# Kernel optimization log

Measured on AMD Instinct MI355X. Metric: run time of the kernel, lower is better.

The kernel has to match this reference:

```python
import jax, jax.numpy as jnp
import numpy as np

K_UP = 5
UP = 2
KS = 3
C_IN = 256


def pixel_shuffle(x, r):
    N, C, H, W = x.shape
    x = x.reshape(N, C // (r * r), r, r, H, W)
    return x.transpose(0, 1, 4, 2, 5, 3).reshape(N, C // (r * r), H * r, W * r)


def conv2d(x, w, b, pad):
    y = jax.lax.conv_general_dilated(
        x, w, window_strides=(1, 1), padding=[(pad, pad), (pad, pad)],
        dimension_numbers=('NCHW', 'OIHW', 'NCHW'))
    return y + b[None, :, None, None]


def setup_inputs() -> dict:
    key = jax.random.key(0)
    ks = jax.random.split(key, 7)
    C = C_IN
    Cd = C // 2
    Ce = UP * UP * K_UP * K_UP  # 100
    x = jax.random.normal(ks[0], (4, C, 64, 64), dtype=jnp.float32)
    # kaiming-normal-ish inits, biases small uniform (torch default)
    w_down = jax.random.normal(ks[1], (Cd, C, 1, 1), dtype=jnp.float32) * np.sqrt(2.0 / C)
    b_down = jax.random.uniform(ks[2], (Cd,), dtype=jnp.float32, minval=-0.05, maxval=0.05)
    w_enc = jax.random.normal(ks[3], (Ce, Cd, KS, KS), dtype=jnp.float32) * np.sqrt(2.0 / (Cd * KS * KS))
    b_enc = jax.random.uniform(ks[4], (Ce,), dtype=jnp.float32, minval=-0.05, maxval=0.05)
    w_out = jax.random.normal(ks[5], (C, C, 1, 1), dtype=jnp.float32) * np.sqrt(2.0 / C)
    b_out = jax.random.uniform(ks[6], (C,), dtype=jnp.float32, minval=-0.05, maxval=0.05)
    return {"x": x, "w_down": w_down, "b_down": b_down, "w_enc": w_enc,
            "b_enc": b_enc, "w_out": w_out, "b_out": b_out}


def reference(x, w_down, b_down, w_enc, b_enc, w_out, b_out):
    N, C, H, W = x.shape
    k2 = K_UP * K_UP  # 25
    u2 = UP * UP      # 4
    # kernel prediction branch
    kt = conv2d(x, w_down, b_down, 0)
    kt = conv2d(kt, w_enc, b_enc, KS // 2)
    kt = pixel_shuffle(kt, UP)              # (N, 25, H*UP, W*UP)
    kt = jax.nn.softmax(kt, axis=1)
    # unfold(2,UP,UP).unfold(3,UP,UP) -> (N,25,H,W,UP,UP) -> (N,H,W,25,UP*UP)
    kt = kt.reshape(N, k2, H, UP, W, UP).transpose(0, 2, 4, 1, 3, 5)
    kt = kt.reshape(N, H, W, k2, u2)
    # feature patches: pad then gather k_up x k_up window per pixel
    pad = K_UP // 2
    xp = jnp.pad(x, ((0, 0), (0, 0), (pad, pad), (pad, pad)))
    patches = jnp.stack(
        [xp[:, :, i:i + H, j:j + W] for i in range(K_UP) for j in range(K_UP)],
        axis=-1)                            # (N, C, H, W, 25)
    # per-pixel weighted sum: (N,H,W,C,25) @ (N,H,W,25,u2)
    out = jnp.einsum('nchwk,nhwkp->nchwp', patches, kt)  # (N,C,H,W,u2)
    out = out.transpose(0, 1, 4, 2, 3).reshape(N, C * u2, H, W)
    out = pixel_shuffle(out, UP)            # (N, C, H*UP, W*UP)
    return conv2d(out, w_out, b_out, 0)
```

## Files before the change

kernel.cpp:

```cpp
#include <hip/hip_runtime.h>
#include <hip/hip_bf16.h>


#define NB    4
#define NPIX  4096

typedef short s16x8 __attribute__((ext_vector_type(8)));
typedef float f32x4 __attribute__((ext_vector_type(4)));

#define MFMA16(a, b, c) __builtin_amdgcn_mfma_f32_16x16x32_bf16((a), (b), (c), 0, 0, 0)

__device__ __forceinline__ ushort f2b(float f) {
    __hip_bfloat16 h = __float2bfloat16(f);
    return *(ushort*)&h;
}
__device__ __forceinline__ float b2f(ushort u) {
    unsigned v = ((unsigned)u) << 16;
    return *(float*)&v;
}

__global__ __launch_bounds__(256) void prep_kernel(
    const float* __restrict__ wd, const float* __restrict__ wo,
    const float* __restrict__ we,
    ushort* __restrict__ wcomb, ushort* __restrict__ wrb)
{
    int idx = blockIdx.x * 256 + threadIdx.x;
    if (idx < 98304) {
        float v = (idx < 32768) ? wd[idx] : wo[idx - 32768];
        wcomb[idx] = f2b(v);
    } else if (idx < 227328) {
        int i = idx - 98304;
        int co = i / 1152, k = i - co * 1152;
        int tap = k >> 7, c = k & 127;
        float v = (co < 100) ? we[(co * 128 + c) * 9 + tap] : 0.0f;
        wrb[i] = f2b(v);
    }
}

__global__ __launch_bounds__(512, 1) void dual_gemm_kernel(
    const float*  __restrict__ X,
    const ushort* __restrict__ Wcomb,
    const float*  __restrict__ b_down,
    ushort* __restrict__ T1t,
    ushort* __restrict__ XOt)
{
    __shared__ __attribute__((aligned(16))) ushort xs[64][264];
    const int n = blockIdx.y, p0 = blockIdx.x * 64;
    const int tid = threadIdx.x, lane = tid & 63, wid = tid >> 6;
    const int l15 = lane & 15, l4 = lane >> 4;
    const float* Xn = X + (size_t)n * 256 * NPIX + p0;

    {
        int c = tid >> 1, half = tid & 1;
        const float* src = Xn + (size_t)c * NPIX + half * 32;
        #pragma unroll
        for (int j = 0; j < 8; j++) {
            float4 v = *(const float4*)&src[j * 4];
            int pix = half * 32 + j * 4;
            xs[pix + 0][c] = f2b(v.x);
            xs[pix + 1][c] = f2b(v.y);
            xs[pix + 2][c] = f2b(v.z);
            xs[pix + 3][c] = f2b(v.w);
        }
    }
    __syncthreads();

    const int wp = wid >> 1;
    const int wc = wid & 1;
    const int crow = wc * 192;

    f32x4 acc[12] = {};
    #pragma unroll
    for (int ks = 0; ks < 8; ks++) {
        int k0 = ks * 32 + l4 * 8;
        s16x8 a = *(const s16x8*)&xs[wp * 16 + l15][k0];
        #pragma unroll
        for (int cf = 0; cf < 12; cf++) {
            s16x8 b = *(const s16x8*)&Wcomb[(size_t)(crow + cf * 16 + l15) * 256 + k0];
            acc[cf] = MFMA16(a, b, acc[cf]);
        }
    }

    #pragma unroll
    for (int cf = 0; cf < 12; cf++) {
        int cbase = crow + cf * 16;
        int c = cbase + l15;
        if (cbase < 128) {
            float bb = b_down[c];
            #pragma unroll
            for (int r = 0; r < 4; r++) {
                int pix = p0 + wp * 16 + l4 * 4 + r;
                T1t[(size_t)(n * NPIX + pix) * 128 + c] = f2b(acc[cf][r] + bb);
            }
        } else {
            int c2 = c - 128;
            #pragma unroll
            for (int r = 0; r < 4; r++) {
                int pix = p0 + wp * 16 + l4 * 4 + r;
                XOt[(size_t)(n * NPIX + pix) * 256 + c2] = f2b(acc[cf][r]);
            }
        }
    }
}

#define SMEM_A 27264
#define SMEM_TOTAL (SMEM_A + 74240)

__global__ __launch_bounds__(512, 1) void carafe_fused_kernel(
    const ushort* __restrict__ T1t,
    const ushort* __restrict__ Wr,
    const float*  __restrict__ Benc,
    const ushort* __restrict__ XOt,
    const float*  __restrict__ Bout,
    float* __restrict__ Z)
{
    __shared__ __attribute__((aligned(16))) char smem[SMEM_TOTAL];
    ushort (*hs)[136]   = (ushort(*)[136])smem;
    float  (*sm)[64][4] = (float(*)[64][4])smem;
    float  (*eld)[101]  = (float(*)[101])(smem + SMEM_A);
    float  (*xs)[145]   = (float(*)[145])(smem + SMEM_A);

    const int n = blockIdx.y, tile = blockIdx.x;
    const int h0 = (tile >> 3) * 8, w0 = (tile & 7) * 8;
    const int tid = threadIdx.x, lane = tid & 63, wid = tid >> 6;
    const int l15 = lane & 15, l4 = lane >> 4;

    for (int u = tid; u < 1600; u += 512) {
        int hp = u >> 4, ch = u & 15;
        int r = hp / 10, s = hp - r * 10;
        int gh = h0 - 1 + r, gw = w0 - 1 + s;
        s16x8 v = {};
        if ((unsigned)gh < 64u && (unsigned)gw < 64u)
            v = *(const s16x8*)&T1t[((size_t)n * NPIX + gh * 64 + gw) * 128 + ch * 8];
        *(s16x8*)&hs[hp][ch * 8] = v;
    }
    __syncthreads();

    if (wid < 4) {
        const int pl = wid * 16 + l15;
        const int ph = pl >> 3, pw = pl & 7;
        f32x4 acc[7] = {};
        for (int tap = 0; tap < 9; tap++) {
            int dy = tap / 3, dx = tap - dy * 3;
            int hp = (ph + dy) * 10 + pw + dx;
            const ushort* hrow = &hs[hp][l4 * 8];
            const ushort* wrow = &Wr[(size_t)l15 * 1152 + tap * 128 + l4 * 8];
            #pragma unroll
            for (int cb = 0; cb < 4; cb++) {
                s16x8 b = *(const s16x8*)&hrow[cb * 32];
                #pragma unroll
                for (int mf = 0; mf < 7; mf++) {
                    s16x8 a = *(const s16x8*)&wrow[(size_t)mf * 16 * 1152 + cb * 32];
                    acc[mf] = MFMA16(a, b, acc[mf]);
                }
            }
        }
        #pragma unroll
        for (int mf = 0; mf < 7; mf++) {
            #pragma unroll
            for (int r = 0; r < 4; r++) {
                int co = mf * 16 + l4 * 4 + r;
                if (co < 100) eld[pl][co] = acc[mf][r] + Benc[co];
            }
        }
    }
    __syncthreads();

    if (tid < 256) {
        int p = tid & 3, pix = tid >> 2;
        float v[25];
        float mx = -1e30f;
        #pragma unroll
        for (int k = 0; k < 25; k++) { v[k] = eld[pix][4 * k + p]; mx = fmaxf(mx, v[k]); }
        float ssum = 0.0f;
        #pragma unroll
        for (int k = 0; k < 25; k++) { v[k] = __expf(v[k] - mx); ssum += v[k]; }
        float inv = 1.0f / ssum;
        #pragma unroll
        for (int k = 0; k < 25; k++) sm[k][pix][p] = v[k] * inv;
    }
    __syncthreads();

    const int pix = tid & 63;
    const int og8 = tid >> 6;
    const int ph = pix >> 3, pw = pix & 7;
    const int cl = og8 >> 2;
    const int g  = og8 & 3;

    for (int it = 0; it < 2; it++) {
        for (int u = tid; u < 4608; u += 512) {
            int hp = u >> 5, cg = u & 31;
            int r = hp / 12, s = hp - r * 12;
            int gh = h0 - 2 + r, gw = w0 - 2 + s;
            float v0 = 0.f, v1 = 0.f, v2 = 0.f, v3 = 0.f;
            if ((unsigned)gh < 64u && (unsigned)gw < 64u) {
                ushort4 raw = *(const ushort4*)&XOt[((size_t)n * NPIX + gh * 64 + gw) * 256 + it * 128 + cg * 4];
                v0 = b2f(raw.x); v1 = b2f(raw.y); v2 = b2f(raw.z); v3 = b2f(raw.w);
            }
            xs[cg * 4 + 0][hp] = v0;
            xs[cg * 4 + 1][hp] = v1;
            xs[cg * 4 + 2][hp] = v2;
            xs[cg * 4 + 3][hp] = v3;
        }
        __syncthreads();

        float acc[16][4] = {};
        for (int k = 0; k < 25; k++) {
            int di = k / 5, dj = k - di * 5;
            float4 wv = *(const float4*)&sm[k][pix][0];
            int base = (ph + di) * 12 + pw + dj;
            #pragma unroll
            for (int i = 0; i < 16; i++) {
                float xv = xs[cl * 64 + g * 16 + i][base];
                acc[i][0] += xv * wv.x;
                acc[i][1] += xv * wv.y;
                acc[i][2] += xv * wv.z;
                acc[i][3] += xv * wv.w;
            }
        }

        const int gh = h0 + ph, gw = w0 + pw;
        const int oc = it * 2 + cl;
        #pragma unroll
        for (int i = 0; i < 16; i++) {
            int o = oc * 64 + g * 16 + i;
            float bb = Bout[o];
            float2 r0 = make_float2(acc[i][0] + bb, acc[i][1] + bb);
            float2 r1 = make_float2(acc[i][2] + bb, acc[i][3] + bb);
            size_t zb = (((size_t)n * 256 + o) * 128 + 2 * gh) * 128 + 2 * gw;
            *(float2*)&Z[zb]       = r0;
            *(float2*)&Z[zb + 128] = r1;
        }
        if (it == 0) __syncthreads();
    }
}

extern "C" void kernel_launch(void* const* d_in, const int* in_sizes, int n_in,
                              void* d_out, int out_size, void* d_ws, size_t ws_size,
                              hipStream_t stream) {
    const float* x      = (const float*)d_in[0];
    const float* w_down = (const float*)d_in[1];
    const float* b_down = (const float*)d_in[2];
    const float* w_enc  = (const float*)d_in[3];
    const float* b_enc  = (const float*)d_in[4];
    const float* w_out  = (const float*)d_in[5];
    const float* b_out  = (const float*)d_in[6];
    float* z = (float*)d_out;

    ushort* t1T   = (ushort*)d_ws;
    ushort* xoT   = t1T + 2097152;
    ushort* wcomb = xoT + 4194304;
    ushort* wrb   = wcomb + 98304;

    prep_kernel<<<888, 256, 0, stream>>>(w_down, w_out, w_enc, wcomb, wrb);
    dual_gemm_kernel<<<dim3(64, NB), 512, 0, stream>>>(x, wcomb, b_down, t1T, xoT);
    carafe_fused_kernel<<<dim3(64, NB), 512, 0, stream>>>(t1T, wrb, b_enc, xoT, b_out, z);
}
```

Before: 170.1 us.

## Split fused CARAFE kernel into conv-softmax and reassembly kernels for more blocks

The fused conv+softmax+reassembly kernel becomes two kernels: one computes the encoder conv and softmax and writes the softmax weights to global workspace, the other does the reassembly per 64-channel group over a 3D grid of 1024 blocks. The dual GEMM kernel is also retiled to 32-pixel, 256-thread blocks with two blocks per CU. The aim is to fill the GPU, since the old grid of 256 blocks of 512 threads left many CUs idle on this chip. In exchange it adds a global round trip for the softmax weights, an extra launch, and repeated loads of the weights by each channel group.

```diff
diff --git a/kernel.cpp b/kernel.cpp
--- a/kernel.cpp
+++ b/kernel.cpp
@@ -37,40 +37,37 @@
     }
 }
 
-__global__ __launch_bounds__(512, 1) void dual_gemm_kernel(
+__global__ __launch_bounds__(256, 2) void dual_gemm_kernel(
     const float*  __restrict__ X,
     const ushort* __restrict__ Wcomb,
     const float*  __restrict__ b_down,
     ushort* __restrict__ T1t,
     ushort* __restrict__ XOt)
 {
-    __shared__ __attribute__((aligned(16))) ushort xs[64][264];
-    const int n = blockIdx.y, p0 = blockIdx.x * 64;
+    __shared__ __attribute__((aligned(16))) ushort xs[32][264];
+    const int n = blockIdx.y, p0 = blockIdx.x * 32;
     const int tid = threadIdx.x, lane = tid & 63, wid = tid >> 6;
     const int l15 = lane & 15, l4 = lane >> 4;
-    const float* Xn = X + (size_t)n * 256 * NPIX + p0;
-
-    {
-        int c = tid >> 1, half = tid & 1;
-        const float* src = Xn + (size_t)c * NPIX + half * 32;
+
+    {
+        const float* src = X + (size_t)n * 256 * NPIX + (size_t)tid * NPIX + p0;
         #pragma unroll
         for (int j = 0; j < 8; j++) {
             float4 v = *(const float4*)&src[j * 4];
-            int pix = half * 32 + j * 4;
-            xs[pix + 0][c] = f2b(v.x);
-            xs[pix + 1][c] = f2b(v.y);
-            xs[pix + 2][c] = f2b(v.z);
-            xs[pix + 3][c] = f2b(v.w);
-        }
-    }
-    __syncthreads();
-
-    const int wp = wid >> 1;
-    const int wc = wid & 1;
+            xs[j * 4 + 0][tid] = f2b(v.x);
+            xs[j * 4 + 1][tid] = f2b(v.y);
+            xs[j * 4 + 2][tid] = f2b(v.z);
+            xs[j * 4 + 3][tid] = f2b(v.w);
+        }
+    }
+    __syncthreads();
+
+    const int wp = wid & 1;
+    const int wc = wid >> 1;
     const int crow = wc * 192;
 
     f32x4 acc[12] = {};
-    #pragma unroll
+    #pragma unroll 2
     for (int ks = 0; ks < 8; ks++) {
         int k0 = ks * 32 + l4 * 8;
         s16x8 a = *(const s16x8*)&xs[wp * 16 + l15][k0];
@@ -103,29 +100,21 @@
     }
 }
 
-#define SMEM_A 27264
-#define SMEM_TOTAL (SMEM_A + 74240)
-
-__global__ __launch_bounds__(512, 1) void carafe_fused_kernel(
+__global__ __launch_bounds__(256, 3) void conv_sm_kernel(
     const ushort* __restrict__ T1t,
     const ushort* __restrict__ Wr,
     const float*  __restrict__ Benc,
-    const ushort* __restrict__ XOt,
-    const float*  __restrict__ Bout,
-    float* __restrict__ Z)
-{
-    __shared__ __attribute__((aligned(16))) char smem[SMEM_TOTAL];
-    ushort (*hs)[136]   = (ushort(*)[136])smem;
-    float  (*sm)[64][4] = (float(*)[64][4])smem;
-    float  (*eld)[101]  = (float(*)[101])(smem + SMEM_A);
-    float  (*xs)[145]   = (float(*)[145])(smem + SMEM_A);
+    float* __restrict__ SMg)
+{
+    __shared__ __attribute__((aligned(16))) ushort hs[100][136];
+    __shared__ float eld[64][101];
 
     const int n = blockIdx.y, tile = blockIdx.x;
     const int h0 = (tile >> 3) * 8, w0 = (tile & 7) * 8;
     const int tid = threadIdx.x, lane = tid & 63, wid = tid >> 6;
     const int l15 = lane & 15, l4 = lane >> 4;
 
-    for (int u = tid; u < 1600; u += 512) {
+    for (int u = tid; u < 1600; u += 256) {
         int hp = u >> 4, ch = u & 15;
         int r = hp / 10, s = hp - r * 10;
         int gh = h0 - 1 + r, gw = w0 - 1 + s;
@@ -136,7 +125,7 @@
     }
     __syncthreads();
 
-    if (wid < 4) {
+    {
         const int pl = wid * 16 + l15;
         const int ph = pl >> 3, pw = pl & 7;
         f32x4 acc[7] = {};
@@ -166,7 +155,7 @@
     }
     __syncthreads();
 
-    if (tid < 256) {
+    {
         int p = tid & 3, pix = tid >> 2;
         float v[25];
         float mx = -1e30f;
@@ -176,62 +165,78 @@
         #pragma unroll
         for (int k = 0; k < 25; k++) { v[k] = __expf(v[k] - mx); ssum += v[k]; }
         float inv = 1.0f / ssum;
-        #pragma unroll
-        for (int k = 0; k < 25; k++) sm[k][pix][p] = v[k] * inv;
+        float* dst = SMg + (size_t)(n * 64 + tile) * 6400;
+        #pragma unroll
+        for (int k = 0; k < 25; k++)
+            dst[k * 256 + tid] = v[k] * inv;
+    }
+}
+
+__global__ __launch_bounds__(256, 2) void reassembly_kernel(
+    const float*  __restrict__ SMg,
+    const ushort* __restrict__ XOt,
+    const float*  __restrict__ Bout,
+    float* __restrict__ Z)
+{
+    __shared__ __attribute__((aligned(16))) float sml[6400];
+    __shared__ float xs[64][145];
+
+    const int tile = blockIdx.x, oc = blockIdx.y, n = blockIdx.z;
+    const int h0 = (tile >> 3) * 8, w0 = (tile & 7) * 8;
+    const int tid = threadIdx.x;
+
+    {
+        const float* src = SMg + (size_t)(n * 64 + tile) * 6400;
+        #pragma unroll
+        for (int j = 0; j < 25; j++)
+            sml[j * 256 + tid] = src[j * 256 + tid];
+    }
+
+    for (int u = tid; u < 2304; u += 256) {
+        int hp = u >> 4, cg = u & 15;
+        int r = hp / 12, s = hp - r * 12;
+        int gh = h0 - 2 + r, gw = w0 - 2 + s;
+        float v0 = 0.f, v1 = 0.f, v2 = 0.f, v3 = 0.f;
+        if ((unsigned)gh < 64u && (unsigned)gw < 64u) {
+            ushort4 raw = *(const ushort4*)&XOt[((size_t)n * NPIX + gh * 64 + gw) * 256 + oc * 64 + cg * 4];
+            v0 = b2f(raw.x); v1 = b2f(raw.y); v2 = b2f(raw.z); v3 = b2f(raw.w);
+        }
+        xs[cg * 4 + 0][hp] = v0;
+        xs[cg * 4 + 1][hp] = v1;
+        xs[cg * 4 + 2][hp] = v2;
+        xs[cg * 4 + 3][hp] = v3;
     }
     __syncthreads();
 
     const int pix = tid & 63;
-    const int og8 = tid >> 6;
+    const int og = tid >> 6;
     const int ph = pix >> 3, pw = pix & 7;
-    const int cl = og8 >> 2;
-    const int g  = og8 & 3;
-
-    for (int it = 0; it < 2; it++) {
-        for (int u = tid; u < 4608; u += 512) {
-            int hp = u >> 5, cg = u & 31;
-            int r = hp / 12, s = hp - r * 12;
-            int gh = h0 - 2 + r, gw = w0 - 2 + s;
-            float v0 = 0.f, v1 = 0.f, v2 = 0.f, v3 = 0.f;
-            if ((unsigned)gh < 64u && (unsigned)gw < 64u) {
-                ushort4 raw = *(const ushort4*)&XOt[((size_t)n * NPIX + gh * 64 + gw) * 256 + it * 128 + cg * 4];
-                v0 = b2f(raw.x); v1 = b2f(raw.y); v2 = b2f(raw.z); v3 = b2f(raw.w);
-            }
-            xs[cg * 4 + 0][hp] = v0;
-            xs[cg * 4 + 1][hp] = v1;
-            xs[cg * 4 + 2][hp] = v2;
-            xs[cg * 4 + 3][hp] = v3;
-        }
-        __syncthreads();
-
-        float acc[16][4] = {};
-        for (int k = 0; k < 25; k++) {
-            int di = k / 5, dj = k - di * 5;
-            float4 wv = *(const float4*)&sm[k][pix][0];
-            int base = (ph + di) * 12 + pw + dj;
-            #pragma unroll
-            for (int i = 0; i < 16; i++) {
-                float xv = xs[cl * 64 + g * 16 + i][base];
-                acc[i][0] += xv * wv.x;
-                acc[i][1] += xv * wv.y;
-                acc[i][2] += xv * wv.z;
-                acc[i][3] += xv * wv.w;
-            }
-        }
-
-        const int gh = h0 + ph, gw = w0 + pw;
-        const int oc = it * 2 + cl;
+
+    float acc[16][4] = {};
+    for (int k = 0; k < 25; k++) {
+        int di = k / 5, dj = k - di * 5;
+        float4 wv = *(const float4*)&sml[k * 256 + pix * 4];
+        int base = (ph + di) * 12 + pw + dj;
         #pragma unroll
         for (int i = 0; i < 16; i++) {
-            int o = oc * 64 + g * 16 + i;
-            float bb = Bout[o];
-            float2 r0 = make_float2(acc[i][0] + bb, acc[i][1] + bb);
-            float2 r1 = make_float2(acc[i][2] + bb, acc[i][3] + bb);
-            size_t zb = (((size_t)n * 256 + o) * 128 + 2 * gh) * 128 + 2 * gw;
-            *(float2*)&Z[zb]       = r0;
-            *(float2*)&Z[zb + 128] = r1;
-        }
-        if (it == 0) __syncthreads();
+            float xv = xs[og * 16 + i][base];
+            acc[i][0] += xv * wv.x;
+            acc[i][1] += xv * wv.y;
+            acc[i][2] += xv * wv.z;
+            acc[i][3] += xv * wv.w;
+        }
+    }
+
+    const int gh = h0 + ph, gw = w0 + pw;
+    #pragma unroll
+    for (int i = 0; i < 16; i++) {
+        int o = oc * 64 + og * 16 + i;
+        float bb = Bout[o];
+        float2 r0 = make_float2(acc[i][0] + bb, acc[i][1] + bb);
+        float2 r1 = make_float2(acc[i][2] + bb, acc[i][3] + bb);
+        size_t zb = (((size_t)n * 256 + o) * 128 + 2 * gh) * 128 + 2 * gw;
+        *(float2*)&Z[zb]       = r0;
+        *(float2*)&Z[zb + 128] = r1;
     }
 }
 
@@ -251,8 +256,10 @@
     ushort* xoT   = t1T + 2097152;
     ushort* wcomb = xoT + 4194304;
     ushort* wrb   = wcomb + 98304;
+    float*  smg   = (float*)(wrb + 129024);
 
     prep_kernel<<<888, 256, 0, stream>>>(w_down, w_out, w_enc, wcomb, wrb);
-    dual_gemm_kernel<<<dim3(64, NB), 512, 0, stream>>>(x, wcomb, b_down, t1T, xoT);
-    carafe_fused_kernel<<<dim3(64, NB), 512, 0, stream>>>(t1T, wrb, b_enc, xoT, b_out, z);
-}
+    dual_gemm_kernel<<<dim3(128, NB), 256, 0, stream>>>(x, wcomb, b_down, t1T, xoT);
+    conv_sm_kernel<<<dim3(64, NB), 256, 0, stream>>>(t1T, wrb, b_enc, smg);
+    reassembly_kernel<<<dim3(64, 4, NB), 256, 0, stream>>>(smg, xoT, b_out, z);
+}
```

New measurement: 175.9 us. 3.4% more time.
